# Optimization experiments

Measured on AMD Instinct MI355X. Metric: run time of the kernel, lower is better.

## Reference

```python
import jax, jax.numpy as jnp
import numpy as np

TOP_K = 8

def setup_inputs() -> dict:
    key = jax.random.key(0)
    k1, k2 = jax.random.split(key)
    hidden_states = jax.random.normal(k1, (4, 4096, 2048), dtype=jnp.float32)
    weight = jax.random.normal(k2, (64, 2048), dtype=jnp.float32) * 0.02
    return {"hidden_states": hidden_states, "weight": weight}

def reference(hidden_states, weight):
    b, s, h = hidden_states.shape
    x = hidden_states.reshape(-1, h).astype(jnp.float32)   # [T, H]
    logits = jnp.einsum('th,eh->te', x, weight.astype(jnp.float32))  # [T, E]
    scores = jax.nn.softmax(logits, axis=-1)               # greedy router: softmax then top-k
    topk_weights, topk_idx = jax.lax.top_k(scores, TOP_K)  # [T, k]
    # renormalize top-k probabilities (norm_topk_prob)
    topk_weights = topk_weights / jnp.sum(topk_weights, axis=-1, keepdims=True)
    return topk_weights, topk_idx
```

## Files before the change

### kernel.cpp

```cpp
#include <hip/hip_runtime.h>
#include <math.h>


#define H_DIM 2048
#define N_EXP 64
#define TOPK 8
#define TOK 64
#define NW 8
#define KSL (H_DIM / NW)
#define CH 16
#define NIT (KSL / CH)
#define XBUF 4096
#define WBUF 4096

__global__ __launch_bounds__(512, 2) void moe_gate_kernel(
    const float* __restrict__ x, const float* __restrict__ w,
    float* __restrict__ out, int n_tokens) {
  __shared__ float lds[32768];
  char* const ldsb = (char*)lds;

  const int tid = threadIdx.x;
  const int l = tid & 63;
  const int wave = tid >> 6;
  const int kh = __builtin_amdgcn_readfirstlane(wave);
  const int t0 = blockIdx.x * TOK;

  char* const xbase = ldsb + kh * (2 * XBUF);
  char* const wbase = ldsb + 65536 + kh * (2 * WBUF);

  const int tr = l >> 3;
  const int er = l & 7;
  const int xsw = tr & 3;
  const int wsw = er & 3;

  const int lr4 = l >> 2;
  const char* gxp[4];
  const char* gwp[4];
#pragma unroll
  for (int j = 0; j < 4; ++j) {
    const int row = j * 16 + lr4;
    const int g = (l & 3) ^ ((2 * j + (l >> 5)) & 3);
    gxp[j] = (const char*)(x + (size_t)(t0 + row) * H_DIM + kh * KSL) + g * 16;
    gwp[j] = (const char*)(w + (size_t)row * H_DIM + kh * KSL) + g * 16;
  }

  float acc[8][8];
#pragma unroll
  for (int a = 0; a < 8; ++a)
#pragma unroll
    for (int b = 0; b < 8; ++b) acc[a][b] = 0.f;

  auto stage = [&](int ii) {
    char* xb = xbase + (ii & 1) * XBUF;
    char* wb = wbase + (ii & 1) * WBUF;
#pragma unroll
    for (int j = 0; j < 4; ++j) {
      __builtin_amdgcn_global_load_lds(
          (const __attribute__((address_space(1))) void*)(gxp[j] +
                                                          ii * (CH * 4)),
          (__attribute__((address_space(3))) void*)(xb + j * 1024), 16, 0, 0);
      __builtin_amdgcn_global_load_lds(
          (const __attribute__((address_space(1))) void*)(gwp[j] +
                                                          ii * (CH * 4)),
          (__attribute__((address_space(3))) void*)(wb + j * 1024), 16, 0, 0);
    }
  };

  stage(0);

#pragma unroll 1
  for (int i = 0; i < NIT; ++i) {
    if (i + 1 < NIT) {
      stage(i + 1);
      asm volatile("s_waitcnt vmcnt(8)" ::: "memory");
    } else {
      asm volatile("s_waitcnt vmcnt(0)" ::: "memory");
    }
    __builtin_amdgcn_sched_barrier(0);

    const char* xr = xbase + (i & 1) * XBUF + (tr * 8) * 64;
    const char* wr = wbase + (i & 1) * WBUF + (er * 8) * 64;
#pragma unroll
    for (int c = 0; c < 4; ++c) {
      float4 xv[8], wv[8];
#pragma unroll
      for (int jt = 0; jt < 8; ++jt)
        xv[jt] =
            *reinterpret_cast<const float4*>(xr + jt * 64 + ((c ^ xsw) << 4));
#pragma unroll
      for (int je = 0; je < 8; ++je)
        wv[je] =
            *reinterpret_cast<const float4*>(wr + je * 64 + ((c ^ wsw) << 4));
#pragma unroll
      for (int jt = 0; jt < 8; ++jt)
#pragma unroll
        for (int je = 0; je < 8; ++je) {
          acc[jt][je] = fmaf(xv[jt].x, wv[je].x, acc[jt][je]);
          acc[jt][je] = fmaf(xv[jt].y, wv[je].y, acc[jt][je]);
          acc[jt][je] = fmaf(xv[jt].z, wv[je].z, acc[jt][je]);
          acc[jt][je] = fmaf(xv[jt].w, wv[je].w, acc[jt][je]);
        }
    }
  }

  __syncthreads();
  for (int z = tid; z < N_EXP * TOK; z += 512) lds[z] = 0.f;
  __syncthreads();
#pragma unroll
  for (int jt = 0; jt < 8; ++jt)
#pragma unroll
    for (int je = 0; je < 8; ++je)
      atomicAdd(&lds[(er * 8 + je) * TOK + (tr * 8 + jt)], acc[jt][je]);
  __syncthreads();

  if (wave != 0) return;

  float lg[N_EXP];
#pragma unroll
  for (int e = 0; e < N_EXP; ++e) lg[e] = lds[e * TOK + l];

  float bw[TOPK];
  int bi[TOPK];
#pragma unroll
  for (int k = 0; k < TOPK; ++k) {
    float m = lg[0];
    int mi = 0;
#pragma unroll
    for (int e = 1; e < N_EXP; ++e) {
      if (lg[e] > m) {
        m = lg[e];
        mi = e;
      }
    }
    bw[k] = m;
    bi[k] = mi;
#pragma unroll
    for (int e = 0; e < N_EXP; ++e)
      if (e == mi) lg[e] = -INFINITY;
  }

  const float mx = bw[0];
  float ew[TOPK];
  float s = 0.f;
#pragma unroll
  for (int k = 0; k < TOPK; ++k) {
    ew[k] = expf(bw[k] - mx);
    s += ew[k];
  }
  const float inv = 1.f / s;

  float4 w0, w1, i0, i1;
  w0.x = ew[0] * inv; w0.y = ew[1] * inv; w0.z = ew[2] * inv; w0.w = ew[3] * inv;
  w1.x = ew[4] * inv; w1.y = ew[5] * inv; w1.z = ew[6] * inv; w1.w = ew[7] * inv;
  i0.x = (float)bi[0]; i0.y = (float)bi[1]; i0.z = (float)bi[2]; i0.w = (float)bi[3];
  i1.x = (float)bi[4]; i1.y = (float)bi[5]; i1.z = (float)bi[6]; i1.w = (float)bi[7];

  const int t = t0 + l;
  float4* ow = reinterpret_cast<float4*>(out + (size_t)t * TOPK);
  ow[0] = w0;
  ow[1] = w1;
  float4* oi =
      reinterpret_cast<float4*>(out + (size_t)n_tokens * TOPK + (size_t)t * TOPK);
  oi[0] = i0;
  oi[1] = i1;
}

extern "C" void kernel_launch(void* const* d_in, const int* in_sizes, int n_in,
                              void* d_out, int out_size, void* d_ws,
                              size_t ws_size, hipStream_t stream) {
  const float* x = (const float*)d_in[0];
  const float* w = (const float*)d_in[1];
  float* out = (float*)d_out;
  const int n_tokens = in_sizes[0] / H_DIM;
  const int n_blocks = n_tokens / TOK;
  moe_gate_kernel<<<n_blocks, 512, 0, stream>>>(x, w, out, n_tokens);
}
```

Before: 264.0 us.

## Halve token tile, triple-buffer LDS staging, replace atomic reduction with partial sums

The token tile per block drops from 64 to 32, the per-thread accumulator shrinks to 4x8, and LDS use is cut so that four blocks can fit per CU instead of two. The K-chunk per stage is halved and loads become triple-buffered with a prefetch distance of two, using new swizzled layouts. The cross-wave reduction moves from LDS float atomics to per-wave partial buffers summed in a fixed order. The cost is twice as many blocks, each re-reading the full weight matrix, which doubles weight traffic.

```diff
diff --git a/kernel.cpp b/kernel.cpp
--- a/kernel.cpp
+++ b/kernel.cpp
@@ -5,18 +5,19 @@
 #define H_DIM 2048
 #define N_EXP 64
 #define TOPK 8
-#define TOK 64
+#define TOK 32
 #define NW 8
 #define KSL (H_DIM / NW)
-#define CH 16
+#define CH 8
 #define NIT (KSL / CH)
-#define XBUF 4096
-#define WBUF 4096
+#define XCH 1024
+#define WCH 2048
+#define WREG (3 * (XCH + WCH))
 
-__global__ __launch_bounds__(512, 2) void moe_gate_kernel(
+__global__ __launch_bounds__(512, 4) void moe_gate_kernel(
     const float* __restrict__ x, const float* __restrict__ w,
     float* __restrict__ out, int n_tokens) {
-  __shared__ float lds[32768];
+  __shared__ float lds[18432];
   char* const ldsb = (char*)lds;
 
   const int tid = threadIdx.x;
@@ -25,74 +26,76 @@
   const int kh = __builtin_amdgcn_readfirstlane(wave);
   const int t0 = blockIdx.x * TOK;
 
-  char* const xbase = ldsb + kh * (2 * XBUF);
-  char* const wbase = ldsb + 65536 + kh * (2 * WBUF);
+  char* const wreg = ldsb + kh * WREG;
+
+  const int sc = l >> 5;
+  const int sr = l & 31;
+  const int stok = (sr & 24) | ((sr & 7) ^ ((sr >> 3) & 3));
+  const float* gx = x + (size_t)(t0 + stok) * H_DIM + kh * KSL + sc * 4;
+  const int serw = (l >> 3) & 7;
+  const int sje = (l & 7) ^ serw;
+  const float* gwr = w + (size_t)(serw * 8 + sje) * H_DIM + kh * KSL;
 
   const int tr = l >> 3;
   const int er = l & 7;
-  const int xsw = tr & 3;
-  const int wsw = er & 3;
+  int xg[4], wg[8];
+#pragma unroll
+  for (int jt = 0; jt < 4; ++jt) {
+    const int tok = tr * 4 + jt;
+    xg[jt] = ((tok & 24) | ((tok & 7) ^ ((tok >> 3) & 3))) << 4;
+  }
+#pragma unroll
+  for (int je = 0; je < 8; ++je) wg[je] = (er * 8 + (je ^ er)) << 4;
 
-  const int lr4 = l >> 2;
-  const char* gxp[4];
-  const char* gwp[4];
+  float acc[4][8];
 #pragma unroll
-  for (int j = 0; j < 4; ++j) {
-    const int row = j * 16 + lr4;
-    const int g = (l & 3) ^ ((2 * j + (l >> 5)) & 3);
-    gxp[j] = (const char*)(x + (size_t)(t0 + row) * H_DIM + kh * KSL) + g * 16;
-    gwp[j] = (const char*)(w + (size_t)row * H_DIM + kh * KSL) + g * 16;
-  }
-
-  float acc[8][8];
-#pragma unroll
-  for (int a = 0; a < 8; ++a)
+  for (int a = 0; a < 4; ++a)
 #pragma unroll
     for (int b = 0; b < 8; ++b) acc[a][b] = 0.f;
 
-  auto stage = [&](int ii) {
-    char* xb = xbase + (ii & 1) * XBUF;
-    char* wb = wbase + (ii & 1) * WBUF;
-#pragma unroll
-    for (int j = 0; j < 4; ++j) {
-      __builtin_amdgcn_global_load_lds(
-          (const __attribute__((address_space(1))) void*)(gxp[j] +
-                                                          ii * (CH * 4)),
-          (__attribute__((address_space(3))) void*)(xb + j * 1024), 16, 0, 0);
-      __builtin_amdgcn_global_load_lds(
-          (const __attribute__((address_space(1))) void*)(gwp[j] +
-                                                          ii * (CH * 4)),
-          (__attribute__((address_space(3))) void*)(wb + j * 1024), 16, 0, 0);
-    }
+  auto stage = [&](int ii, int xo, int wo) {
+    __builtin_amdgcn_global_load_lds(
+        (const __attribute__((address_space(1))) void*)(gx + ii * CH),
+        (__attribute__((address_space(3))) void*)(wreg + xo), 16, 0, 0);
+    __builtin_amdgcn_global_load_lds(
+        (const __attribute__((address_space(1))) void*)(gwr + ii * CH),
+        (__attribute__((address_space(3))) void*)(wreg + wo), 16, 0, 0);
+    __builtin_amdgcn_global_load_lds(
+        (const __attribute__((address_space(1))) void*)(gwr + ii * CH + 4),
+        (__attribute__((address_space(3))) void*)(wreg + wo + 1024), 16, 0, 0);
   };
 
-  stage(0);
+  int xo0 = 0, xo1 = 1024, xo2 = 2048;
+  int wo0 = 3072, wo1 = 5120, wo2 = 7168;
+
+  stage(0, xo0, wo0);
+  stage(1, xo1, wo1);
 
 #pragma unroll 1
   for (int i = 0; i < NIT; ++i) {
-    if (i + 1 < NIT) {
-      stage(i + 1);
-      asm volatile("s_waitcnt vmcnt(8)" ::: "memory");
+    if (i + 2 < NIT) {
+      stage(i + 2, xo2, wo2);
+      asm volatile("s_waitcnt vmcnt(6)" ::: "memory");
+    } else if (i + 1 < NIT) {
+      asm volatile("s_waitcnt vmcnt(3)" ::: "memory");
     } else {
       asm volatile("s_waitcnt vmcnt(0)" ::: "memory");
     }
     __builtin_amdgcn_sched_barrier(0);
 
-    const char* xr = xbase + (i & 1) * XBUF + (tr * 8) * 64;
-    const char* wr = wbase + (i & 1) * WBUF + (er * 8) * 64;
+    const char* xb = wreg + xo0;
+    const char* wb = wreg + wo0;
 #pragma unroll
-    for (int c = 0; c < 4; ++c) {
-      float4 xv[8], wv[8];
+    for (int c = 0; c < 2; ++c) {
+      float4 xv[4], wv[8];
 #pragma unroll
-      for (int jt = 0; jt < 8; ++jt)
-        xv[jt] =
-            *reinterpret_cast<const float4*>(xr + jt * 64 + ((c ^ xsw) << 4));
+      for (int jt = 0; jt < 4; ++jt)
+        xv[jt] = *reinterpret_cast<const float4*>(xb + c * 512 + xg[jt]);
 #pragma unroll
       for (int je = 0; je < 8; ++je)
-        wv[je] =
-            *reinterpret_cast<const float4*>(wr + je * 64 + ((c ^ wsw) << 4));
+        wv[je] = *reinterpret_cast<const float4*>(wb + c * 1024 + wg[je]);
 #pragma unroll
-      for (int jt = 0; jt < 8; ++jt)
+      for (int jt = 0; jt < 4; ++jt)
 #pragma unroll
         for (int je = 0; je < 8; ++je) {
           acc[jt][je] = fmaf(xv[jt].x, wv[je].x, acc[jt][je]);
@@ -101,23 +104,37 @@
           acc[jt][je] = fmaf(xv[jt].w, wv[je].w, acc[jt][je]);
         }
     }
+    int tx = xo0; xo0 = xo1; xo1 = xo2; xo2 = tx;
+    int tw = wo0; wo0 = wo1; wo1 = wo2; wo2 = tw;
   }
 
   __syncthreads();
-  for (int z = tid; z < N_EXP * TOK; z += 512) lds[z] = 0.f;
+  float* part = lds;
+#pragma unroll
+  for (int je = 0; je < 8; ++je) {
+    float4 v;
+    v.x = acc[0][je];
+    v.y = acc[1][je];
+    v.z = acc[2][je];
+    v.w = acc[3][je];
+    *reinterpret_cast<float4*>(part + kh * (N_EXP * TOK) +
+                               (er * 8 + je) * TOK + tr * 4) = v;
+  }
   __syncthreads();
-#pragma unroll
-  for (int jt = 0; jt < 8; ++jt)
-#pragma unroll
-    for (int je = 0; je < 8; ++je)
-      atomicAdd(&lds[(er * 8 + je) * TOK + (tr * 8 + jt)], acc[jt][je]);
+  float* logits = lds + NW * N_EXP * TOK;
+  for (int z = tid; z < N_EXP * TOK; z += 512) {
+    float s = ((part[z] + part[2048 + z]) + (part[4096 + z] + part[6144 + z])) +
+              ((part[8192 + z] + part[10240 + z]) +
+               (part[12288 + z] + part[14336 + z]));
+    logits[z] = s;
+  }
   __syncthreads();
 
-  if (wave != 0) return;
+  if (tid >= TOK) return;
 
   float lg[N_EXP];
 #pragma unroll
-  for (int e = 0; e < N_EXP; ++e) lg[e] = lds[e * TOK + l];
+  for (int e = 0; e < N_EXP; ++e) lg[e] = logits[e * TOK + tid];
 
   float bw[TOPK];
   int bi[TOPK];
@@ -155,7 +172,7 @@
   i0.x = (float)bi[0]; i0.y = (float)bi[1]; i0.z = (float)bi[2]; i0.w = (float)bi[3];
   i1.x = (float)bi[4]; i1.y = (float)bi[5]; i1.z = (float)bi[6]; i1.w = (float)bi[7];
 
-  const int t = t0 + l;
+  const int t = t0 + tid;
   float4* ow = reinterpret_cast<float4*>(out + (size_t)t * TOPK);
   ow[0] = w0;
   ow[1] = w1;
```

New measurement: 259.7 us. No clear change (-1.6%).
